# Kernel tuning notes

Measured on AMD Instinct MI355X. Metric: run time of the kernel, lower is better.

The kernel has to match this reference:

```python
import jax, jax.numpy as jnp
import numpy as np

U, I, D, OUT = 8192, 16384, 64, 64

def setup_inputs() -> dict:
    key = jax.random.key(0)
    k1, k2, k3, k4 = jax.random.split(key, 4)
    user_emb = jax.random.normal(k1, (U, D), dtype=jnp.float32)
    item_emb = jax.random.normal(k2, (I, D), dtype=jnp.float32)
    attention_weight = jax.random.normal(k3, (D, OUT), dtype=jnp.float32) * (1.0 / np.sqrt(D))
    adj_matrix = jax.random.randint(k4, (U, I), 0, 2, dtype=jnp.int32)
    return {"user_emb": user_emb, "item_emb": item_emb,
            "attention_weight": attention_weight, "adj_matrix": adj_matrix}

def reference(user_emb, item_emb, attention_weight, adj_matrix):
    # score[u,i] = <user_emb[u], item_emb[i]>  (torch.inner)
    score = jnp.einsum('ud,id->ui', user_emb, item_emb)
    # mask non-edges to 0 (NOT -inf, faithful to torch.where(adj>0, score, 0))
    score = jnp.where(adj_matrix > 0, score, 0.0)
    score = jax.nn.softmax(score, axis=1)
    # flag == True path: aggregate items into users, then project
    output = score @ item_emb          # [U, D]
    output = output @ attention_weight  # [U, OUT]
    return output
```

## Files before the change

kernel.cpp:

```cpp
#include <hip/hip_runtime.h>
#include <hip/hip_bf16.h>
#include <math.h>

#define U_N   8192
#define I_N   16384
#define D_N   64
#define OUT_N 64
#define BN    32
#define PL_ST 40

typedef _Float16       half8  __attribute__((ext_vector_type(8)));
typedef short          bf16x8 __attribute__((ext_vector_type(8)));
typedef float          f32x4  __attribute__((ext_vector_type(4)));

static __device__ __forceinline__ unsigned short f2bf(float f) {
    union { __hip_bfloat16 h; unsigned short u; } cv;
    cv.h = __float2bfloat16(f);
    return cv.u;
}

static __device__ __forceinline__ float rsum16(float v) {
    #pragma unroll
    for (int o = 1; o < 16; o <<= 1) v += __shfl_xor(v, o);
    return v;
}

__global__ __launch_bounds__(256)
void prep_items(const float* __restrict__ item,
                _Float16* __restrict__ itemH,
                unsigned short* __restrict__ itemT)
{
    const int i = blockIdx.x * 256 + threadIdx.x;
    const float* src = item + (size_t)i * D_N;
    f32x4 v[16];
    #pragma unroll
    for (int j = 0; j < 16; ++j) v[j] = *(const f32x4*)(src + 4 * j);

    #pragma unroll
    for (int j = 0; j < 8; ++j) {
        half8 h;
        #pragma unroll
        for (int k = 0; k < 4; ++k) { h[k] = (_Float16)v[2*j][k]; h[4+k] = (_Float16)v[2*j+1][k]; }
        *(half8*)&itemH[(size_t)i * D_N + 8 * j] = h;
    }
    #pragma unroll
    for (int d = 0; d < 64; ++d)
        itemT[(size_t)d * I_N + i] = f2bf(v[d >> 2][d & 3]);
}

#define DECL_BUF(BUF) \
    int   adj##BUF##0, adj##BUF##1, adj##BUF##2, adj##BUF##3, \
          adj##BUF##4, adj##BUF##5, adj##BUF##6, adj##BUF##7; \
    half8 sb##BUF##0, sb##BUF##1, sb##BUF##2, sb##BUF##3;

#define PREFETCH(BUF, it_) do { \
    const size_t off_ = (size_t)(it_) * BN; \
    adj##BUF##0 = adjb[0 * (size_t)I_N + off_ +  0]; \
    adj##BUF##1 = adjb[0 * (size_t)I_N + off_ + 16]; \
    adj##BUF##2 = adjb[1 * (size_t)I_N + off_ +  0]; \
    adj##BUF##3 = adjb[1 * (size_t)I_N + off_ + 16]; \
    adj##BUF##4 = adjb[2 * (size_t)I_N + off_ +  0]; \
    adj##BUF##5 = adjb[2 * (size_t)I_N + off_ + 16]; \
    adj##BUF##6 = adjb[3 * (size_t)I_N + off_ +  0]; \
    adj##BUF##7 = adjb[3 * (size_t)I_N + off_ + 16]; \
    sb##BUF##0 = *(const half8*)&sbb[(off_ +  0) * D_N +  0]; \
    sb##BUF##1 = *(const half8*)&sbb[(off_ +  0) * D_N + 32]; \
    sb##BUF##2 = *(const half8*)&sbb[(off_ + 16) * D_N +  0]; \
    sb##BUF##3 = *(const half8*)&sbb[(off_ + 16) * D_N + 32]; \
} while (0)

#define COMPUTE(BUF, it_) do { \
    const size_t off_ = (size_t)(it_) * BN; \
    bf16x8 pv0_ = *(const bf16x8*)&pvb[ 0 * (size_t)I_N + off_]; \
    bf16x8 pv1_ = *(const bf16x8*)&pvb[16 * (size_t)I_N + off_]; \
    bf16x8 pv2_ = *(const bf16x8*)&pvb[32 * (size_t)I_N + off_]; \
    bf16x8 pv3_ = *(const bf16x8*)&pvb[48 * (size_t)I_N + off_]; \
    f32x4 S0_ = (f32x4){0.f,0.f,0.f,0.f}; \
    f32x4 S1_ = (f32x4){0.f,0.f,0.f,0.f}; \
    S0_ = __builtin_amdgcn_mfma_f32_16x16x32_f16(ufrag0, sb##BUF##0, S0_, 0, 0, 0); \
    S0_ = __builtin_amdgcn_mfma_f32_16x16x32_f16(ufrag1, sb##BUF##1, S0_, 0, 0, 0); \
    S1_ = __builtin_amdgcn_mfma_f32_16x16x32_f16(ufrag0, sb##BUF##2, S1_, 0, 0, 0); \
    S1_ = __builtin_amdgcn_mfma_f32_16x16x32_f16(ufrag1, sb##BUF##3, S1_, 0, 0, 0); \
    float e_; \
    e_ = __expf((adj##BUF##0 != 0) ? S0_[0] : 0.0f); S0_[0] = e_; l0 += e_; \
    e_ = __expf((adj##BUF##1 != 0) ? S1_[0] : 0.0f); S1_[0] = e_; l0 += e_; \
    e_ = __expf((adj##BUF##2 != 0) ? S0_[1] : 0.0f); S0_[1] = e_; l1 += e_; \
    e_ = __expf((adj##BUF##3 != 0) ? S1_[1] : 0.0f); S1_[1] = e_; l1 += e_; \
    e_ = __expf((adj##BUF##4 != 0) ? S0_[2] : 0.0f); S0_[2] = e_; l2 += e_; \
    e_ = __expf((adj##BUF##5 != 0) ? S1_[2] : 0.0f); S1_[2] = e_; l2 += e_; \
    e_ = __expf((adj##BUF##6 != 0) ? S0_[3] : 0.0f); S0_[3] = e_; l3 += e_; \
    e_ = __expf((adj##BUF##7 != 0) ? S1_[3] : 0.0f); S1_[3] = e_; l3 += e_; \
    plw[(4*q+0)*PL_ST +  0 + c] = f2bf(S0_[0]); \
    plw[(4*q+0)*PL_ST + 16 + c] = f2bf(S1_[0]); \
    plw[(4*q+1)*PL_ST +  0 + c] = f2bf(S0_[1]); \
    plw[(4*q+1)*PL_ST + 16 + c] = f2bf(S1_[1]); \
    plw[(4*q+2)*PL_ST +  0 + c] = f2bf(S0_[2]); \
    plw[(4*q+2)*PL_ST + 16 + c] = f2bf(S1_[2]); \
    plw[(4*q+3)*PL_ST +  0 + c] = f2bf(S0_[3]); \
    plw[(4*q+3)*PL_ST + 16 + c] = f2bf(S1_[3]); \
    bf16x8 pf_ = *(const bf16x8*)&plw[c * PL_ST + q * 8]; \
    O0 = __builtin_amdgcn_mfma_f32_16x16x32_bf16(pf_, pv0_, O0, 0, 0, 0); \
    O1 = __builtin_amdgcn_mfma_f32_16x16x32_bf16(pf_, pv1_, O1, 0, 0, 0); \
    O2 = __builtin_amdgcn_mfma_f32_16x16x32_bf16(pf_, pv2_, O2, 0, 0, 0); \
    O3 = __builtin_amdgcn_mfma_f32_16x16x32_bf16(pf_, pv3_, O3, 0, 0, 0); \
} while (0)

__global__ __launch_bounds__(256, 3)
void atten_main(const float* __restrict__ user_emb,
                const _Float16* __restrict__ itemH,
                const unsigned short* __restrict__ itemT,
                const int*   __restrict__ adj,
                float* __restrict__ wsO,
                float* __restrict__ wsL,
                int items_per_ch, int iters)
{
    __shared__ unsigned short Pl[4][16 * PL_ST];

    const int ch   = blockIdx.x;
    const int ub   = blockIdx.y;
    const int t    = threadIdx.x;
    const int w    = t >> 6;
    const int lane = t & 63;
    const int c    = lane & 15;
    const int q    = lane >> 4;

    const int urow0  = ub * 64 + w * 16;
    const int ibase0 = ch * items_per_ch;

    unsigned short* plw = &Pl[w][0];

    half8 ufrag0, ufrag1;
    {
        const float* up = user_emb + (size_t)(urow0 + c) * D_N + q * 8;
        f32x4 a0 = *(const f32x4*)(up);
        f32x4 b0 = *(const f32x4*)(up + 4);
        f32x4 a1 = *(const f32x4*)(up + 32);
        f32x4 b1 = *(const f32x4*)(up + 36);
        #pragma unroll
        for (int j = 0; j < 4; ++j) {
            ufrag0[j] = (_Float16)a0[j]; ufrag0[4 + j] = (_Float16)b0[j];
            ufrag1[j] = (_Float16)a1[j]; ufrag1[4 + j] = (_Float16)b1[j];
        }
    }

    f32x4 O0 = (f32x4){0.f,0.f,0.f,0.f};
    f32x4 O1 = O0, O2 = O0, O3 = O0;
    float l0 = 0.f, l1 = 0.f, l2 = 0.f, l3 = 0.f;

    const int*            adjb = adj   + (size_t)(urow0 + 4 * q) * I_N + ibase0 + c;
    const _Float16*       sbb  = itemH + (size_t)(ibase0 + c) * D_N + q * 8;
    const unsigned short* pvb  = itemT + (size_t)c * I_N + ibase0 + q * 8;

    DECL_BUF(A)
    DECL_BUF(B)

    PREFETCH(A, 0);
    PREFETCH(B, 1);

    int it = 0;
    for (; it < iters - 2; it += 2) {
        COMPUTE(A, it);
        PREFETCH(A, it + 2);
        COMPUTE(B, it + 1);
        PREFETCH(B, it + 3);
    }
    COMPUTE(A, iters - 2);
    COMPUTE(B, iters - 1);

    l0 = rsum16(l0); l1 = rsum16(l1); l2 = rsum16(l2); l3 = rsum16(l3);

    {
        float* d0 = wsO + ((size_t)ch * U_N + urow0 + 4 * q + 0) * D_N;
        float* d1 = wsO + ((size_t)ch * U_N + urow0 + 4 * q + 1) * D_N;
        float* d2 = wsO + ((size_t)ch * U_N + urow0 + 4 * q + 2) * D_N;
        float* d3 = wsO + ((size_t)ch * U_N + urow0 + 4 * q + 3) * D_N;
        d0[c] = O0[0]; d0[16 + c] = O1[0]; d0[32 + c] = O2[0]; d0[48 + c] = O3[0];
        d1[c] = O0[1]; d1[16 + c] = O1[1]; d1[32 + c] = O2[1]; d1[48 + c] = O3[1];
        d2[c] = O0[2]; d2[16 + c] = O1[2]; d2[32 + c] = O2[2]; d2[48 + c] = O3[2];
        d3[c] = O0[3]; d3[16 + c] = O1[3]; d3[32 + c] = O2[3]; d3[48 + c] = O3[3];
    }
    if (c == 0) {
        float* lw = wsL + (size_t)ch * U_N + urow0 + 4 * q;
        lw[0] = l0; lw[1] = l1; lw[2] = l2; lw[3] = l3;
    }
}

__global__ __launch_bounds__(256)
void atten_combine(const float* __restrict__ wsO,
                   const float* __restrict__ wsL,
                   const float* __restrict__ attw,
                   float* __restrict__ out,
                   int nch)
{
    __shared__ float inv[64];
    __shared__ float agg[64][68];
    __shared__ float Wl[64][68];

    const int t  = threadIdx.x;
    const int u0 = blockIdx.x * 64;

    {
        const int d = t >> 2, o0 = (t & 3) * 16;
        const float* src = attw + d * OUT_N + o0;
        #pragma unroll
        for (int j = 0; j < 4; ++j)
            *(f32x4*)&Wl[d][o0 + 4 * j] = *(const f32x4*)(src + 4 * j);
    }
    if (t < 64) {
        float L = 0.f;
        for (int cc = 0; cc < nch; ++cc) L += wsL[(size_t)cc * U_N + u0 + t];
        inv[t] = 1.0f / L;
    }
    __syncthreads();

    {
        const int ul = t >> 2, d0 = (t & 3) * 16;
        const int u = u0 + ul;
        f32x4 a4[4];
        #pragma unroll
        for (int j = 0; j < 4; ++j) a4[j] = (f32x4){0.f, 0.f, 0.f, 0.f};
        for (int cc = 0; cc < nch; ++cc) {
            const float* src = wsO + ((size_t)cc * U_N + u) * D_N + d0;
            #pragma unroll
            for (int j = 0; j < 4; ++j) a4[j] += *(const f32x4*)(src + 4 * j);
        }
        const float s = inv[ul];
        #pragma unroll
        for (int j = 0; j < 4; ++j)
            *(f32x4*)&agg[ul][d0 + 4 * j] = a4[j] * s;
    }
    __syncthreads();

    {
        const int ul = t >> 2, o0 = (t & 3) * 16;
        f32x4 acc[4];
        #pragma unroll
        for (int j = 0; j < 4; ++j) acc[j] = (f32x4){0.f, 0.f, 0.f, 0.f};
        for (int d = 0; d < 64; ++d) {
            const float av = agg[ul][d];
            #pragma unroll
            for (int j = 0; j < 4; ++j) {
                f32x4 wv = *(const f32x4*)&Wl[d][o0 + 4 * j];
                acc[j] += wv * av;
            }
        }
        float* dst = out + (size_t)(u0 + ul) * OUT_N + o0;
        #pragma unroll
        for (int j = 0; j < 4; ++j)
            *(f32x4*)(dst + 4 * j) = acc[j];
    }
}

extern "C" void kernel_launch(void* const* d_in, const int* in_sizes, int n_in,
                              void* d_out, int out_size, void* d_ws, size_t ws_size,
                              hipStream_t stream)
{
    const float* user_emb = (const float*)d_in[0];
    const float* item_emb = (const float*)d_in[1];
    const float* attw     = (const float*)d_in[2];
    const int*   adj      = (const int*)d_in[3];
    float* out = (float*)d_out;

    const int nch = 8;

    float*          wsO   = (float*)d_ws;
    float*          wsL   = wsO + (size_t)nch * U_N * D_N;
    _Float16*       itemH = (_Float16*)(wsL + (size_t)nch * U_N);
    unsigned short* itemT = (unsigned short*)(itemH + (size_t)I_N * D_N);

    const int items_per_ch = I_N / nch;
    const int iters = items_per_ch / BN;

    prep_items<<<dim3(I_N / 256), 256, 0, stream>>>(item_emb, itemH, itemT);
    atten_main<<<dim3(nch, U_N / 64), 256, 0, stream>>>(user_emb, itemH, itemT, adj,
                                                        wsO, wsL, items_per_ch, iters);
    atten_combine<<<dim3(U_N / 64), 256, 0, stream>>>(wsO, wsL, attw, out, nch);
}
```

Before: 839.0 us.

## Stage item tiles cooperatively in double-buffered LDS shared across waves

Before, each wave loaded its own item-embedding fragments (row-major fp16 and transposed bf16) straight from global memory. Now the block loads each 32-item tile once into double-buffered shared memory and all four waves read from it, with a barrier after every tile. The transposed item copy is re-laid out in 32-item blocks so each tile is one contiguous chunk. This cuts redundant global and L2 traffic by a factor of four, at the cost of per-tile barriers, extra LDS use that may lower occupancy, and the adjacency mask being folded into a bitmask.

```diff
diff --git a/kernel.cpp b/kernel.cpp
--- a/kernel.cpp
+++ b/kernel.cpp
@@ -7,28 +7,35 @@
 #define D_N   64
 #define OUT_N 64
 #define BN    32
+#define NCH   8
+#define ITERS 64
+#define VN_ST 72
+#define VT_ST 36
 #define PL_ST 40
 
-typedef _Float16       half8  __attribute__((ext_vector_type(8)));
-typedef short          bf16x8 __attribute__((ext_vector_type(8)));
-typedef float          f32x4  __attribute__((ext_vector_type(4)));
+typedef _Float16 half8  __attribute__((ext_vector_type(8)));
+typedef short    bf16x8 __attribute__((ext_vector_type(8)));
+typedef short    bf16x4 __attribute__((ext_vector_type(4)));
+typedef float    f32x4  __attribute__((ext_vector_type(4)));
 
 static __device__ __forceinline__ unsigned short f2bf(float f) {
     union { __hip_bfloat16 h; unsigned short u; } cv;
     cv.h = __float2bfloat16(f);
     return cv.u;
 }
-
 static __device__ __forceinline__ float rsum16(float v) {
     #pragma unroll
     for (int o = 1; o < 16; o <<= 1) v += __shfl_xor(v, o);
     return v;
 }
+static __device__ __forceinline__ void bar() {
+    asm volatile("s_waitcnt lgkmcnt(0)\n\ts_barrier" ::: "memory");
+}
 
 __global__ __launch_bounds__(256)
 void prep_items(const float* __restrict__ item,
                 _Float16* __restrict__ itemH,
-                unsigned short* __restrict__ itemT)
+                unsigned short* __restrict__ itemTt)
 {
     const int i = blockIdx.x * 256 + threadIdx.x;
     const float* src = item + (size_t)i * D_N;
@@ -43,77 +50,107 @@
         for (int k = 0; k < 4; ++k) { h[k] = (_Float16)v[2*j][k]; h[4+k] = (_Float16)v[2*j+1][k]; }
         *(half8*)&itemH[(size_t)i * D_N + 8 * j] = h;
     }
+    const size_t tb = (size_t)(i >> 5) * (D_N * 32) + (i & 31);
     #pragma unroll
     for (int d = 0; d < 64; ++d)
-        itemT[(size_t)d * I_N + i] = f2bf(v[d >> 2][d & 3]);
-}
-
-#define DECL_BUF(BUF) \
-    int   adj##BUF##0, adj##BUF##1, adj##BUF##2, adj##BUF##3, \
-          adj##BUF##4, adj##BUF##5, adj##BUF##6, adj##BUF##7; \
-    half8 sb##BUF##0, sb##BUF##1, sb##BUF##2, sb##BUF##3;
-
-#define PREFETCH(BUF, it_) do { \
-    const size_t off_ = (size_t)(it_) * BN; \
-    adj##BUF##0 = adjb[0 * (size_t)I_N + off_ +  0]; \
-    adj##BUF##1 = adjb[0 * (size_t)I_N + off_ + 16]; \
-    adj##BUF##2 = adjb[1 * (size_t)I_N + off_ +  0]; \
-    adj##BUF##3 = adjb[1 * (size_t)I_N + off_ + 16]; \
-    adj##BUF##4 = adjb[2 * (size_t)I_N + off_ +  0]; \
-    adj##BUF##5 = adjb[2 * (size_t)I_N + off_ + 16]; \
-    adj##BUF##6 = adjb[3 * (size_t)I_N + off_ +  0]; \
-    adj##BUF##7 = adjb[3 * (size_t)I_N + off_ + 16]; \
-    sb##BUF##0 = *(const half8*)&sbb[(off_ +  0) * D_N +  0]; \
-    sb##BUF##1 = *(const half8*)&sbb[(off_ +  0) * D_N + 32]; \
-    sb##BUF##2 = *(const half8*)&sbb[(off_ + 16) * D_N +  0]; \
-    sb##BUF##3 = *(const half8*)&sbb[(off_ + 16) * D_N + 32]; \
+        itemTt[tb + (size_t)d * 32] = f2bf(v[d >> 2][d & 3]);
+}
+
+#define DECL_SET(S) \
+    int adj##S##0, adj##S##1, adj##S##2, adj##S##3, \
+        adj##S##4, adj##S##5, adj##S##6, adj##S##7;  \
+    half8 vn##S; bf16x8 vt##S;
+
+#define LOAD_ADJ(S, tidx) do { \
+    const size_t o_ = (size_t)(tidx) * BN; \
+    adj##S##0 = adjb[0 * (size_t)I_N + o_ +  0]; \
+    adj##S##1 = adjb[0 * (size_t)I_N + o_ + 16]; \
+    adj##S##2 = adjb[1 * (size_t)I_N + o_ +  0]; \
+    adj##S##3 = adjb[1 * (size_t)I_N + o_ + 16]; \
+    adj##S##4 = adjb[2 * (size_t)I_N + o_ +  0]; \
+    adj##S##5 = adjb[2 * (size_t)I_N + o_ + 16]; \
+    adj##S##6 = adjb[3 * (size_t)I_N + o_ +  0]; \
+    adj##S##7 = adjb[3 * (size_t)I_N + o_ + 16]; \
 } while (0)
 
-#define COMPUTE(BUF, it_) do { \
-    const size_t off_ = (size_t)(it_) * BN; \
-    bf16x8 pv0_ = *(const bf16x8*)&pvb[ 0 * (size_t)I_N + off_]; \
-    bf16x8 pv1_ = *(const bf16x8*)&pvb[16 * (size_t)I_N + off_]; \
-    bf16x8 pv2_ = *(const bf16x8*)&pvb[32 * (size_t)I_N + off_]; \
-    bf16x8 pv3_ = *(const bf16x8*)&pvb[48 * (size_t)I_N + off_]; \
-    f32x4 S0_ = (f32x4){0.f,0.f,0.f,0.f}; \
-    f32x4 S1_ = (f32x4){0.f,0.f,0.f,0.f}; \
-    S0_ = __builtin_amdgcn_mfma_f32_16x16x32_f16(ufrag0, sb##BUF##0, S0_, 0, 0, 0); \
-    S0_ = __builtin_amdgcn_mfma_f32_16x16x32_f16(ufrag1, sb##BUF##1, S0_, 0, 0, 0); \
-    S1_ = __builtin_amdgcn_mfma_f32_16x16x32_f16(ufrag0, sb##BUF##2, S1_, 0, 0, 0); \
-    S1_ = __builtin_amdgcn_mfma_f32_16x16x32_f16(ufrag1, sb##BUF##3, S1_, 0, 0, 0); \
+#define LOAD_TILE(S, tidx) do { \
+    const size_t o_ = (size_t)(tidx) * BN; \
+    vn##S = *(const half8*)&itemH[(ibase0 + o_ + (t >> 3)) * D_N + (t & 7) * 8]; \
+    vt##S = *(const bf16x8*)&itemTt[((ibase0 + o_) >> 5) * (D_N * 32) \
+                                    + (size_t)(t >> 2) * 32 + (t & 3) * 8]; \
+} while (0)
+
+#define COMMIT(S, bufw) do { \
+    *(half8*)&Vn[bufw][(t >> 3) * VN_ST + (t & 7) * 8] = vn##S; \
+    *(bf16x4*)&Vt[bufw][(t >> 2) * VT_ST + (t & 3) * 8]     = \
+        __builtin_shufflevector(vt##S, vt##S, 0, 1, 2, 3); \
+    *(bf16x4*)&Vt[bufw][(t >> 2) * VT_ST + (t & 3) * 8 + 4] = \
+        __builtin_shufflevector(vt##S, vt##S, 4, 5, 6, 7); \
+} while (0)
+
+#define MASK_OF(S) \
+    (((adj##S##0 != 0) ? 1u : 0u)       | ((adj##S##1 != 0) ? 2u : 0u) | \
+     ((adj##S##2 != 0) ? 4u : 0u)       | ((adj##S##3 != 0) ? 8u : 0u) | \
+     ((adj##S##4 != 0) ? 16u : 0u)      | ((adj##S##5 != 0) ? 32u : 0u) | \
+     ((adj##S##6 != 0) ? 64u : 0u)      | ((adj##S##7 != 0) ? 128u : 0u))
+
+#define COMPUTE_REST(msk, bufr) do { \
+    half8 b00 = *(const half8*)&Vn[bufr][(c)      * VN_ST      + q * 8]; \
+    half8 b01 = *(const half8*)&Vn[bufr][(c)      * VN_ST + 32 + q * 8]; \
+    half8 b10 = *(const half8*)&Vn[bufr][(16 + c) * VN_ST      + q * 8]; \
+    half8 b11 = *(const half8*)&Vn[bufr][(16 + c) * VN_ST + 32 + q * 8]; \
+    f32x4 S0 = (f32x4){0.f,0.f,0.f,0.f}; \
+    f32x4 S1 = (f32x4){0.f,0.f,0.f,0.f}; \
+    S0 = __builtin_amdgcn_mfma_f32_16x16x32_f16(ufrag0, b00, S0, 0, 0, 0); \
+    S0 = __builtin_amdgcn_mfma_f32_16x16x32_f16(ufrag1, b01, S0, 0, 0, 0); \
+    S1 = __builtin_amdgcn_mfma_f32_16x16x32_f16(ufrag0, b10, S1, 0, 0, 0); \
+    S1 = __builtin_amdgcn_mfma_f32_16x16x32_f16(ufrag1, b11, S1, 0, 0, 0); \
     float e_; \
-    e_ = __expf((adj##BUF##0 != 0) ? S0_[0] : 0.0f); S0_[0] = e_; l0 += e_; \
-    e_ = __expf((adj##BUF##1 != 0) ? S1_[0] : 0.0f); S1_[0] = e_; l0 += e_; \
-    e_ = __expf((adj##BUF##2 != 0) ? S0_[1] : 0.0f); S0_[1] = e_; l1 += e_; \
-    e_ = __expf((adj##BUF##3 != 0) ? S1_[1] : 0.0f); S1_[1] = e_; l1 += e_; \
-    e_ = __expf((adj##BUF##4 != 0) ? S0_[2] : 0.0f); S0_[2] = e_; l2 += e_; \
-    e_ = __expf((adj##BUF##5 != 0) ? S1_[2] : 0.0f); S1_[2] = e_; l2 += e_; \
-    e_ = __expf((adj##BUF##6 != 0) ? S0_[3] : 0.0f); S0_[3] = e_; l3 += e_; \
-    e_ = __expf((adj##BUF##7 != 0) ? S1_[3] : 0.0f); S1_[3] = e_; l3 += e_; \
-    plw[(4*q+0)*PL_ST +  0 + c] = f2bf(S0_[0]); \
-    plw[(4*q+0)*PL_ST + 16 + c] = f2bf(S1_[0]); \
-    plw[(4*q+1)*PL_ST +  0 + c] = f2bf(S0_[1]); \
-    plw[(4*q+1)*PL_ST + 16 + c] = f2bf(S1_[1]); \
-    plw[(4*q+2)*PL_ST +  0 + c] = f2bf(S0_[2]); \
-    plw[(4*q+2)*PL_ST + 16 + c] = f2bf(S1_[2]); \
-    plw[(4*q+3)*PL_ST +  0 + c] = f2bf(S0_[3]); \
-    plw[(4*q+3)*PL_ST + 16 + c] = f2bf(S1_[3]); \
-    bf16x8 pf_ = *(const bf16x8*)&plw[c * PL_ST + q * 8]; \
-    O0 = __builtin_amdgcn_mfma_f32_16x16x32_bf16(pf_, pv0_, O0, 0, 0, 0); \
-    O1 = __builtin_amdgcn_mfma_f32_16x16x32_bf16(pf_, pv1_, O1, 0, 0, 0); \
-    O2 = __builtin_amdgcn_mfma_f32_16x16x32_bf16(pf_, pv2_, O2, 0, 0, 0); \
-    O3 = __builtin_amdgcn_mfma_f32_16x16x32_bf16(pf_, pv3_, O3, 0, 0, 0); \
+    e_ = __expf(((msk) &   1u) ? S0[0] : 0.0f); S0[0] = e_; l0 += e_; \
+    e_ = __expf(((msk) &   2u) ? S1[0] : 0.0f); S1[0] = e_; l0 += e_; \
+    e_ = __expf(((msk) &   4u) ? S0[1] : 0.0f); S0[1] = e_; l1 += e_; \
+    e_ = __expf(((msk) &   8u) ? S1[1] : 0.0f); S1[1] = e_; l1 += e_; \
+    e_ = __expf(((msk) &  16u) ? S0[2] : 0.0f); S0[2] = e_; l2 += e_; \
+    e_ = __expf(((msk) &  32u) ? S1[2] : 0.0f); S1[2] = e_; l2 += e_; \
+    e_ = __expf(((msk) &  64u) ? S0[3] : 0.0f); S0[3] = e_; l3 += e_; \
+    e_ = __expf(((msk) & 128u) ? S1[3] : 0.0f); S1[3] = e_; l3 += e_; \
+    plw[(4*q+0)*PL_ST +  0 + c] = f2bf(S0[0]); \
+    plw[(4*q+0)*PL_ST + 16 + c] = f2bf(S1[0]); \
+    plw[(4*q+1)*PL_ST +  0 + c] = f2bf(S0[1]); \
+    plw[(4*q+1)*PL_ST + 16 + c] = f2bf(S1[1]); \
+    plw[(4*q+2)*PL_ST +  0 + c] = f2bf(S0[2]); \
+    plw[(4*q+2)*PL_ST + 16 + c] = f2bf(S1[2]); \
+    plw[(4*q+3)*PL_ST +  0 + c] = f2bf(S0[3]); \
+    plw[(4*q+3)*PL_ST + 16 + c] = f2bf(S1[3]); \
+    bf16x8 pf = *(const bf16x8*)&plw[c * PL_ST + q * 8]; \
+    bf16x4 va0 = *(const bf16x4*)&Vt[bufr][(c)      * VT_ST + q * 8]; \
+    bf16x4 vb0 = *(const bf16x4*)&Vt[bufr][(c)      * VT_ST + q * 8 + 4]; \
+    bf16x4 va1 = *(const bf16x4*)&Vt[bufr][(16 + c) * VT_ST + q * 8]; \
+    bf16x4 vb1 = *(const bf16x4*)&Vt[bufr][(16 + c) * VT_ST + q * 8 + 4]; \
+    bf16x4 va2 = *(const bf16x4*)&Vt[bufr][(32 + c) * VT_ST + q * 8]; \
+    bf16x4 vb2 = *(const bf16x4*)&Vt[bufr][(32 + c) * VT_ST + q * 8 + 4]; \
+    bf16x4 va3 = *(const bf16x4*)&Vt[bufr][(48 + c) * VT_ST + q * 8]; \
+    bf16x4 vb3 = *(const bf16x4*)&Vt[bufr][(48 + c) * VT_ST + q * 8 + 4]; \
+    bf16x8 v0 = __builtin_shufflevector(va0, vb0, 0,1,2,3,4,5,6,7); \
+    bf16x8 v1 = __builtin_shufflevector(va1, vb1, 0,1,2,3,4,5,6,7); \
+    bf16x8 v2 = __builtin_shufflevector(va2, vb2, 0,1,2,3,4,5,6,7); \
+    bf16x8 v3 = __builtin_shufflevector(va3, vb3, 0,1,2,3,4,5,6,7); \
+    O0 = __builtin_amdgcn_mfma_f32_16x16x32_bf16(pf, v0, O0, 0, 0, 0); \
+    O1 = __builtin_amdgcn_mfma_f32_16x16x32_bf16(pf, v1, O1, 0, 0, 0); \
+    O2 = __builtin_amdgcn_mfma_f32_16x16x32_bf16(pf, v2, O2, 0, 0, 0); \
+    O3 = __builtin_amdgcn_mfma_f32_16x16x32_bf16(pf, v3, O3, 0, 0, 0); \
 } while (0)
 
 __global__ __launch_bounds__(256, 3)
 void atten_main(const float* __restrict__ user_emb,
                 const _Float16* __restrict__ itemH,
-                const unsigned short* __restrict__ itemT,
+                const unsigned short* __restrict__ itemTt,
                 const int*   __restrict__ adj,
                 float* __restrict__ wsO,
-                float* __restrict__ wsL,
-                int items_per_ch, int iters)
+                float* __restrict__ wsL)
 {
+    __shared__ _Float16 Vn[2][BN * VN_ST];
+    __shared__ short    Vt[2][D_N * VT_ST];
     __shared__ unsigned short Pl[4][16 * PL_ST];
 
     const int ch   = blockIdx.x;
@@ -124,8 +161,8 @@
     const int c    = lane & 15;
     const int q    = lane >> 4;
 
-    const int urow0  = ub * 64 + w * 16;
-    const int ibase0 = ch * items_per_ch;
+    const int    urow0  = ub * 64 + w * 16;
+    const size_t ibase0 = (size_t)ch * (I_N / NCH);
 
     unsigned short* plw = &Pl[w][0];
 
@@ -147,25 +184,39 @@
     f32x4 O1 = O0, O2 = O0, O3 = O0;
     float l0 = 0.f, l1 = 0.f, l2 = 0.f, l3 = 0.f;
 
-    const int*            adjb = adj   + (size_t)(urow0 + 4 * q) * I_N + ibase0 + c;
-    const _Float16*       sbb  = itemH + (size_t)(ibase0 + c) * D_N + q * 8;
-    const unsigned short* pvb  = itemT + (size_t)c * I_N + ibase0 + q * 8;
-
-    DECL_BUF(A)
-    DECL_BUF(B)
-
-    PREFETCH(A, 0);
-    PREFETCH(B, 1);
-
-    int it = 0;
-    for (; it < iters - 2; it += 2) {
-        COMPUTE(A, it);
-        PREFETCH(A, it + 2);
-        COMPUTE(B, it + 1);
-        PREFETCH(B, it + 3);
-    }
-    COMPUTE(A, iters - 2);
-    COMPUTE(B, iters - 1);
+    const int* adjb = adj + (size_t)(urow0 + 4 * q) * I_N + ibase0 + c;
+
+    DECL_SET(A)
+    DECL_SET(B)
+
+    LOAD_TILE(A, 0); LOAD_ADJ(A, 0);
+    LOAD_TILE(B, 1); LOAD_ADJ(B, 1);
+    COMMIT(A, 0);
+    LOAD_TILE(A, 2);
+    bar();
+
+    for (int k = 0; k < ITERS; k += 2) {
+        {
+            const unsigned msk = MASK_OF(A);
+            COMMIT(B, 1);
+            const int ia = (k + 2 < ITERS) ? k + 2 : ITERS - 1;
+            const int iv = (k + 3 < ITERS) ? k + 3 : ITERS - 1;
+            LOAD_ADJ(A, ia);
+            LOAD_TILE(B, iv);
+            COMPUTE_REST(msk, 0);
+            bar();
+        }
+        {
+            const unsigned msk = MASK_OF(B);
+            COMMIT(A, 0);
+            const int ia = (k + 3 < ITERS) ? k + 3 : ITERS - 1;
+            const int iv = (k + 4 < ITERS) ? k + 4 : ITERS - 1;
+            LOAD_ADJ(B, ia);
+            LOAD_TILE(A, iv);
+            COMPUTE_REST(msk, 1);
+            bar();
+        }
+    }
 
     l0 = rsum16(l0); l1 = rsum16(l1); l2 = rsum16(l2); l3 = rsum16(l3);
 
@@ -261,18 +312,13 @@
     const int*   adj      = (const int*)d_in[3];
     float* out = (float*)d_out;
 
-    const int nch = 8;
-
-    float*          wsO   = (float*)d_ws;
-    float*          wsL   = wsO + (size_t)nch * U_N * D_N;
-    _Float16*       itemH = (_Float16*)(wsL + (size_t)nch * U_N);
-    unsigned short* itemT = (unsigned short*)(itemH + (size_t)I_N * D_N);
-
-    const int items_per_ch = I_N / nch;
-    const int iters = items_per_ch / BN;
-
-    prep_items<<<dim3(I_N / 256), 256, 0, stream>>>(item_emb, itemH, itemT);
-    atten_main<<<dim3(nch, U_N / 64), 256, 0, stream>>>(user_emb, itemH, itemT, adj,
-                                                        wsO, wsL, items_per_ch, iters);
-    atten_combine<<<dim3(U_N / 64), 256, 0, stream>>>(wsO, wsL, attw, out, nch);
-}
+    float*          wsO    = (float*)d_ws;
+    float*          wsL    = wsO + (size_t)NCH * U_N * D_N;
+    _Float16*       itemH  = (_Float16*)(wsL + (size_t)NCH * U_N);
+    unsigned short* itemTt = (unsigned short*)(itemH + (size_t)I_N * D_N);
+
+    prep_items<<<dim3(I_N / 256), 256, 0, stream>>>(item_emb, itemH, itemTt);
+    atten_main<<<dim3(NCH, U_N / 64), 256, 0, stream>>>(user_emb, itemH, itemTt, adj,
+                                                        wsO, wsL);
+    atten_combine<<<dim3(U_N / 64), 256, 0, stream>>>(wsO, wsL, attw, out, NCH);
+}
```

Result: faster. 723.8 us (-13.7%).
